# Kernel optimization log

Measured on AMD Instinct MI355X. Metric: run time of the kernel, lower is better.

The kernel has to match this reference:

```python
import jax, jax.numpy as jnp
import numpy as np

B, S, D, F, E, K = 2, 2048, 1024, 4096, 8, 2

def setup_inputs() -> dict:
    key = jax.random.key(0)
    ks = jax.random.split(key, 5)
    x = jax.random.normal(ks[0], (B, S, D), dtype=jnp.float32)
    Wg = jax.random.normal(ks[1], (D, E), dtype=jnp.float32) * 0.02   # gate (fp32)
    W1 = jax.random.normal(ks[2], (E, D, F), dtype=jnp.float32) * 0.02  # expert fc1
    b1 = jnp.zeros((E, F), dtype=jnp.float32)
    W2 = jax.random.normal(ks[3], (E, F, D), dtype=jnp.float32) * 0.02  # expert fc2
    b2 = jnp.zeros((E, D), dtype=jnp.float32)
    return {"x": x, "Wg": Wg, "W1": W1, "b1": b1, "W2": W2, "b2": b2}

def reference(x, Wg, W1, b1, W2, b2):
    b, s, d = x.shape
    e = Wg.shape[1]
    T = b * s
    C = (2 * K * T) // e  # generous capacity -> effectively no token drops
    xt = x.reshape(T, d)

    # --- top-2 gating (fp32) ---
    logits = xt.astype(jnp.float32) @ Wg.astype(jnp.float32)  # [T,E]
    gates = jax.nn.softmax(logits, axis=-1)
    idx1 = jnp.argmax(gates, axis=-1)                      # [T]
    mask1 = jax.nn.one_hot(idx1, e, dtype=gates.dtype)     # [T,E]
    gate1 = jnp.sum(gates * mask1, axis=-1)                # [T]
    logits2 = jnp.where(mask1 > 0, -jnp.inf, logits)
    idx2 = jnp.argmax(logits2, axis=-1)
    mask2 = jax.nn.one_hot(idx2, e, dtype=gates.dtype)
    gate2 = jnp.sum(gates * mask2, axis=-1)
    denom = gate1 + gate2 + 1e-9
    w1 = gate1 / denom
    w2 = gate2 / denom

    # --- capacity-based slot assignment (GShard-style) ---
    p1 = jnp.cumsum(mask1, axis=0) - mask1                 # earlier same-expert tokens
    pos1 = jnp.sum(p1 * mask1, axis=-1).astype(jnp.int32)  # [T]
    off = jnp.sum(mask1, axis=0)                           # [E] 1st-choice counts
    p2 = jnp.cumsum(mask2, axis=0) - mask2 + off[None, :]
    pos2 = jnp.sum(p2 * mask2, axis=-1).astype(jnp.int32)
    keep1 = (pos1 < C).astype(xt.dtype)
    keep2 = (pos2 < C).astype(xt.dtype)
    pos1 = jnp.clip(pos1, 0, C - 1)
    pos2 = jnp.clip(pos2, 0, C - 1)

    # --- dispatch (scatter tokens to expert slots) ---
    xe = jnp.zeros((e, C, d), dtype=xt.dtype)
    xe = xe.at[idx1, pos1].add(xt * keep1[:, None])
    xe = xe.at[idx2, pos2].add(xt * keep2[:, None])

    # --- grouped expert FFN: gelu(x W1 + b1) W2 + b2 ---
    h = jax.nn.gelu(jnp.einsum('ecd,edf->ecf', xe, W1) + b1[:, None, :], approximate=False)
    ye = jnp.einsum('ecf,efd->ecd', h, W2) + b2[:, None, :]  # [E,C,D]

    # --- combine (gather + weighted sum) ---
    out = ye[idx1, pos1] * (w1 * keep1)[:, None] + ye[idx2, pos2] * (w2 * keep2)[:, None]
    return out.reshape(b, s, d)
```

## Files before the change

kernel.cpp:

```cpp
#include <hip/hip_runtime.h>
#include <hip/hip_bf16.h>
#include <math.h>

#define Dv 1024
#define Fv 4096
#define Ev 8
#define Tt 4096
#define CAP 2048

typedef unsigned int u32;
typedef __bf16 bf16x8 __attribute__((ext_vector_type(8)));
typedef float f32x4 __attribute__((ext_vector_type(4)));

__device__ __forceinline__ unsigned short f2bf(float f) {
  u32 u = __float_as_uint(f);
  u32 r = (u + 0x7fffu + ((u >> 16) & 1u)) >> 16;
  return (unsigned short)r;
}

__device__ __forceinline__ void gload_lds16(const void* g, void* l) {
  __builtin_amdgcn_global_load_lds(
      (const __attribute__((address_space(1))) u32*)g,
      (__attribute__((address_space(3))) u32*)l, 16, 0, 0);
}

__global__ void __launch_bounds__(256)
transpose_bf16_kernel(const float* __restrict__ src, unsigned short* __restrict__ dst,
                      int R, int Cc) {
  __shared__ float tile[32][33];
  int e = blockIdx.z;
  src += (size_t)e * R * Cc;
  dst += (size_t)e * R * Cc;
  int c0 = blockIdx.x * 32, r0 = blockIdx.y * 32;
  int tx = threadIdx.x & 31, ty = threadIdx.x >> 5;
#pragma unroll
  for (int i = ty; i < 32; i += 8)
    tile[i][tx] = src[(size_t)(r0 + i) * Cc + (c0 + tx)];
  __syncthreads();
#pragma unroll
  for (int i = ty; i < 32; i += 8)
    dst[(size_t)(c0 + i) * R + (r0 + tx)] = f2bf(tile[tx][i]);
}

__global__ void __launch_bounds__(256)
gating_kernel(const float* __restrict__ x, const float* __restrict__ Wg,
              int* __restrict__ idx1, int* __restrict__ idx2,
              float* __restrict__ w1, float* __restrict__ w2) {
  int t = blockIdx.x * 4 + (threadIdx.x >> 6);
  int lane = threadIdx.x & 63;
  const float* xr = x + (size_t)t * Dv;
  float acc[Ev];
#pragma unroll
  for (int e = 0; e < Ev; ++e) acc[e] = 0.f;
#pragma unroll
  for (int j = 0; j < 4; ++j) {
    int dbase = (lane + 64 * j) * 4;
    float4 xv = *(const float4*)(xr + dbase);
    const float* wr = Wg + (size_t)dbase * Ev;
#pragma unroll
    for (int u = 0; u < 4; ++u) {
      float xd = (&xv.x)[u];
#pragma unroll
      for (int e = 0; e < Ev; ++e) acc[e] += xd * wr[u * Ev + e];
    }
  }
#pragma unroll
  for (int off = 32; off > 0; off >>= 1) {
#pragma unroll
    for (int e = 0; e < Ev; ++e) acc[e] += __shfl_xor(acc[e], off, 64);
  }
  if (lane == 0) {
    float mx = acc[0]; int i1 = 0;
#pragma unroll
    for (int e = 1; e < Ev; ++e) { if (acc[e] > mx) { mx = acc[e]; i1 = e; } }
    float ge[Ev]; float se = 0.f;
#pragma unroll
    for (int e = 0; e < Ev; ++e) { ge[e] = expf(acc[e] - mx); se += ge[e]; }
    float mx2 = -INFINITY; int i2 = 0; bool have = false;
#pragma unroll
    for (int e = 0; e < Ev; ++e) {
      if (e == i1) continue;
      if (!have || acc[e] > mx2) { mx2 = acc[e]; i2 = e; have = true; }
    }
    float g1 = 0.f, g2 = 0.f;
#pragma unroll
    for (int e = 0; e < Ev; ++e) { if (e == i1) g1 = ge[e]; if (e == i2) g2 = ge[e]; }
    g1 /= se; g2 /= se;
    float denom = g1 + g2 + 1e-9f;
    idx1[t] = i1; idx2[t] = i2;
    w1[t] = g1 / denom; w2[t] = g2 / denom;
  }
}

__global__ void __launch_bounds__(256)
scan_kernel(const int* __restrict__ gidx1, const int* __restrict__ gidx2,
            const float* __restrict__ gw1, const float* __restrict__ gw2,
            int* __restrict__ pos1, int* __restrict__ pos2,
            float* __restrict__ w1k, float* __restrict__ w2k,
            int* __restrict__ n_e) {
  __shared__ short s1[Tt], s2[Tt];
  __shared__ int c1[256][Ev], c2[256][Ev];
  __shared__ int tot1[Ev], tot2[Ev];
  int tid = threadIdx.x;
  for (int i = tid; i < Tt; i += 256) { s1[i] = (short)gidx1[i]; s2[i] = (short)gidx2[i]; }
  __syncthreads();
  int base = tid * 16;
  {
    int l1[Ev], l2[Ev];
#pragma unroll
    for (int e = 0; e < Ev; ++e) { l1[e] = 0; l2[e] = 0; }
    for (int j = 0; j < 16; ++j) {
      int a = s1[base + j], b = s2[base + j];
#pragma unroll
      for (int e = 0; e < Ev; ++e) { l1[e] += (a == e); l2[e] += (b == e); }
    }
#pragma unroll
    for (int e = 0; e < Ev; ++e) { c1[tid][e] = l1[e]; c2[tid][e] = l2[e]; }
  }
  __syncthreads();
  if (tid < Ev) {
    int run = 0;
    for (int c = 0; c < 256; ++c) { int v = c1[c][tid]; c1[c][tid] = run; run += v; }
    tot1[tid] = run;
  } else if (tid < 2 * Ev) {
    int e = tid - Ev; int run = 0;
    for (int c = 0; c < 256; ++c) { int v = c2[c][e]; c2[c][e] = run; run += v; }
    tot2[e] = run;
  }
  __syncthreads();
  if (tid < Ev) {
    int ne = tot1[tid] + tot2[tid];
    n_e[tid] = ne < CAP ? ne : CAP;
  }
  int r1[Ev], r2[Ev];
#pragma unroll
  for (int e = 0; e < Ev; ++e) { r1[e] = c1[tid][e]; r2[e] = c2[tid][e] + tot1[e]; }
  for (int j = 0; j < 16; ++j) {
    int tk = base + j;
    int e1 = s1[tk], e2 = s2[tk];
    int p1 = 0, p2 = 0;
#pragma unroll
    for (int e = 0; e < Ev; ++e) {
      if (e == e1) { p1 = r1[e]; r1[e]++; }
      if (e == e2) { p2 = r2[e]; r2[e]++; }
    }
    bool k1 = p1 < CAP, k2 = p2 < CAP;
    pos1[tk] = k1 ? p1 : -1;
    pos2[tk] = k2 ? p2 : -1;
    w1k[tk] = k1 ? gw1[tk] : 0.f;
    w2k[tk] = k2 ? gw2[tk] : 0.f;
  }
}

__global__ void __launch_bounds__(256)
dispatch_kernel(const float* __restrict__ x,
                const int* __restrict__ idx1, const int* __restrict__ idx2,
                const int* __restrict__ pos1, const int* __restrict__ pos2,
                unsigned short* __restrict__ Xe) {
  int t = blockIdx.x, tid = threadIdx.x;
  float4 xv = *(const float4*)(x + (size_t)t * Dv + tid * 4);
  ushort4 bv;
  bv.x = f2bf(xv.x); bv.y = f2bf(xv.y); bv.z = f2bf(xv.z); bv.w = f2bf(xv.w);
  int p1 = pos1[t], p2 = pos2[t];
  int e1 = idx1[t], e2 = idx2[t];
  if (p1 >= 0)
    *(ushort4*)(Xe + ((size_t)(e1 * CAP + p1)) * Dv + tid * 4) = bv;
  if (p2 >= 0)
    *(ushort4*)(Xe + ((size_t)(e2 * CAP + p2)) * Dv + tid * 4) = bv;
}

template <int MODE>
__global__ void __launch_bounds__(256, 2)
gemm_kernel(const unsigned short* __restrict__ A,
            const unsigned short* __restrict__ Bt,
            const float* __restrict__ bias,
            void* __restrict__ Out,
            const int* __restrict__ n_e,
            int M, int N, int K) {
  int e = blockIdx.z;
  int m0 = blockIdx.y * 128, n0 = blockIdx.x * 128;
  if (m0 >= n_e[e]) return;
  A += (size_t)e * M * K;
  Bt += (size_t)e * N * K;
  bias += (size_t)e * N;
  __shared__ unsigned short As[128 * 32];
  __shared__ unsigned short Bs[128 * 32];
  int tid = threadIdx.x;
  int wave = tid >> 6, lane = tid & 63;
  int wm = (wave & 1) * 64, wn = (wave >> 1) * 64;
  int quad = lane >> 4, lr = lane & 15;
  f32x4 acc[4][4];
#pragma unroll
  for (int i = 0; i < 4; ++i)
#pragma unroll
    for (int j = 0; j < 4; ++j)
#pragma unroll
      for (int r = 0; r < 4; ++r) acc[i][j][r] = 0.f;

  int srow = tid >> 2, scol = (tid & 3) * 8;
  const unsigned short* ga = A + (size_t)(m0 + srow) * K + scol;
  const unsigned short* gb = Bt + (size_t)(n0 + srow) * K + scol;
  unsigned short* la = &As[srow * 32 + scol];
  unsigned short* lb = &Bs[srow * 32 + scol];

  for (int k0 = 0; k0 < K; k0 += 32) {
    __syncthreads();
    gload_lds16(ga + k0, la);
    gload_lds16(ga + (size_t)64 * K + k0, la + 64 * 32);
    gload_lds16(gb + k0, lb);
    gload_lds16(gb + (size_t)64 * K + k0, lb + 64 * 32);
    __syncthreads();
    bf16x8 af[4], bfr[4];
#pragma unroll
    for (int mi = 0; mi < 4; ++mi)
      af[mi] = *(const bf16x8*)&As[(wm + mi * 16 + lr) * 32 + quad * 8];
#pragma unroll
    for (int ni = 0; ni < 4; ++ni)
      bfr[ni] = *(const bf16x8*)&Bs[(wn + ni * 16 + lr) * 32 + quad * 8];
#pragma unroll
    for (int mi = 0; mi < 4; ++mi)
#pragma unroll
      for (int ni = 0; ni < 4; ++ni)
        acc[mi][ni] = __builtin_amdgcn_mfma_f32_16x16x32_bf16(af[mi], bfr[ni], acc[mi][ni], 0, 0, 0);
  }

#pragma unroll
  for (int ni = 0; ni < 4; ++ni) {
    int col = n0 + wn + ni * 16 + lr;
    float bv = bias[col];
#pragma unroll
    for (int mi = 0; mi < 4; ++mi) {
#pragma unroll
      for (int r = 0; r < 4; ++r) {
        int row = m0 + wm + mi * 16 + quad * 4 + r;
        float v = acc[mi][ni][r] + bv;
        if (MODE == 0) {
          v = 0.5f * v * (1.0f + erff(v * 0.70710678118654752f));
          ((unsigned short*)Out)[((size_t)e * M + row) * N + col] = f2bf(v);
        } else {
          ((float*)Out)[((size_t)e * M + row) * N + col] = v;
        }
      }
    }
  }
}

__global__ void __launch_bounds__(256)
combine_kernel(const float* __restrict__ ye,
               const int* __restrict__ idx1, const int* __restrict__ idx2,
               const int* __restrict__ pos1, const int* __restrict__ pos2,
               const float* __restrict__ w1k, const float* __restrict__ w2k,
               float* __restrict__ out) {
  int t = blockIdx.x, tid = threadIdx.x;
  int p1 = pos1[t], p2 = pos2[t];
  float a1 = w1k[t], a2 = w2k[t];
  float4 o = make_float4(0.f, 0.f, 0.f, 0.f);
  if (p1 >= 0) {
    float4 y = *(const float4*)(ye + ((size_t)(idx1[t] * CAP + p1)) * Dv + tid * 4);
    o.x += a1 * y.x; o.y += a1 * y.y; o.z += a1 * y.z; o.w += a1 * y.w;
  }
  if (p2 >= 0) {
    float4 y = *(const float4*)(ye + ((size_t)(idx2[t] * CAP + p2)) * Dv + tid * 4);
    o.x += a2 * y.x; o.y += a2 * y.y; o.z += a2 * y.z; o.w += a2 * y.w;
  }
  *(float4*)(out + (size_t)t * Dv + tid * 4) = o;
}

extern "C" void kernel_launch(void* const* d_in, const int* in_sizes, int n_in,
                              void* d_out, int out_size, void* d_ws, size_t ws_size,
                              hipStream_t stream) {
  const float* x  = (const float*)d_in[0];
  const float* Wg = (const float*)d_in[1];
  const float* W1 = (const float*)d_in[2];
  const float* b1 = (const float*)d_in[3];
  const float* W2 = (const float*)d_in[4];
  const float* b2 = (const float*)d_in[5];
  float* out = (float*)d_out;

  char* p = (char*)d_ws;
  size_t off = 0;
  auto alloc = [&](size_t bytes) {
    void* q = p + off;
    off += (bytes + 255) & ~(size_t)255;
    return q;
  };
  unsigned short* Wt1 = (unsigned short*)alloc((size_t)Ev * Fv * Dv * 2);
  unsigned short* Wt2 = (unsigned short*)alloc((size_t)Ev * Dv * Fv * 2);
  unsigned short* Xe  = (unsigned short*)alloc((size_t)Ev * CAP * Dv * 2);
  unsigned short* h   = (unsigned short*)alloc((size_t)Ev * CAP * Fv * 2);
  int*   idx1 = (int*)alloc(Tt * 4);
  int*   idx2 = (int*)alloc(Tt * 4);
  int*   pos1 = (int*)alloc(Tt * 4);
  int*   pos2 = (int*)alloc(Tt * 4);
  float* w1   = (float*)alloc(Tt * 4);
  float* w2   = (float*)alloc(Tt * 4);
  float* w1k  = (float*)alloc(Tt * 4);
  float* w2k  = (float*)alloc(Tt * 4);
  int*   n_e  = (int*)alloc(Ev * 4);
  float* ye   = (float*)Wt1;

  transpose_bf16_kernel<<<dim3(Fv / 32, Dv / 32, Ev), 256, 0, stream>>>(W1, Wt1, Dv, Fv);
  transpose_bf16_kernel<<<dim3(Dv / 32, Fv / 32, Ev), 256, 0, stream>>>(W2, Wt2, Fv, Dv);
  gating_kernel<<<Tt / 4, 256, 0, stream>>>(x, Wg, idx1, idx2, w1, w2);
  scan_kernel<<<1, 256, 0, stream>>>(idx1, idx2, w1, w2, pos1, pos2, w1k, w2k, n_e);
  dispatch_kernel<<<Tt, 256, 0, stream>>>(x, idx1, idx2, pos1, pos2, Xe);
  gemm_kernel<0><<<dim3(Fv / 128, CAP / 128, Ev), 256, 0, stream>>>(
      Xe, Wt1, b1, h, n_e, CAP, Fv, Dv);
  gemm_kernel<1><<<dim3(Dv / 128, CAP / 128, Ev), 256, 0, stream>>>(
      h, Wt2, b2, ye, n_e, CAP, Dv, Fv);
  combine_kernel<<<Tt, 256, 0, stream>>>(ye, idx1, idx2, pos1, pos2, w1k, w2k, out);
}
```

Before: 678.5 us.

## Double GEMM K-tile to 64 with XOR-swizzled LDS and widen transpose tiles

The grouped GEMM now loads a 64-wide K slice per iteration, which halves the number of barrier pairs per K loop. It also XOR-swizzles the LDS column groups so the 128-byte rows avoid bank conflicts on fragment reads. The weight transpose kernel moves to 64x64 tiles and writes paired bf16 values as 32-bit stores, giving wider global writes. LDS use per block doubles to 32KB, which could affect occupancy with two blocks per CU.

New measurement: 622.0 us. 8.3% less time.

```diff
diff --git a/kernel.cpp b/kernel.cpp
--- a/kernel.cpp
+++ b/kernel.cpp
@@ -27,19 +27,25 @@
 __global__ void __launch_bounds__(256)
 transpose_bf16_kernel(const float* __restrict__ src, unsigned short* __restrict__ dst,
                       int R, int Cc) {
-  __shared__ float tile[32][33];
+  __shared__ float tile[64][65];
   int e = blockIdx.z;
   src += (size_t)e * R * Cc;
   dst += (size_t)e * R * Cc;
-  int c0 = blockIdx.x * 32, r0 = blockIdx.y * 32;
-  int tx = threadIdx.x & 31, ty = threadIdx.x >> 5;
-#pragma unroll
-  for (int i = ty; i < 32; i += 8)
-    tile[i][tx] = src[(size_t)(r0 + i) * Cc + (c0 + tx)];
+  int c0 = blockIdx.x * 64, r0 = blockIdx.y * 64;
+  int tc = threadIdx.x & 63, tr = threadIdx.x >> 6;
+#pragma unroll
+  for (int i = tr; i < 64; i += 4)
+    tile[i][tc] = src[(size_t)(r0 + i) * Cc + (c0 + tc)];
   __syncthreads();
-#pragma unroll
-  for (int i = ty; i < 32; i += 8)
-    dst[(size_t)(c0 + i) * R + (r0 + tx)] = f2bf(tile[tx][i]);
+  int rp = (threadIdx.x & 31) * 2, co = threadIdx.x >> 5;
+#pragma unroll
+  for (int k = 0; k < 8; ++k) {
+    int c = co + 8 * k;
+    ushort2 v;
+    v.x = f2bf(tile[rp][c]);
+    v.y = f2bf(tile[rp + 1][c]);
+    *(ushort2*)&dst[(size_t)(c0 + c) * R + (r0 + rp)] = v;
+  }
 }
 
 __global__ void __launch_bounds__(256)
@@ -183,12 +189,13 @@
   A += (size_t)e * M * K;
   Bt += (size_t)e * N * K;
   bias += (size_t)e * N;
-  __shared__ unsigned short As[128 * 32];
-  __shared__ unsigned short Bs[128 * 32];
+  __shared__ unsigned short As[128 * 64];
+  __shared__ unsigned short Bs[128 * 64];
   int tid = threadIdx.x;
   int wave = tid >> 6, lane = tid & 63;
   int wm = (wave & 1) * 64, wn = (wave >> 1) * 64;
   int quad = lane >> 4, lr = lane & 15;
+  int sw = lr & 7;
   f32x4 acc[4][4];
 #pragma unroll
   for (int i = 0; i < 4; ++i)
@@ -197,31 +204,43 @@
 #pragma unroll
       for (int r = 0; r < 4; ++r) acc[i][j][r] = 0.f;
 
-  int srow = tid >> 2, scol = (tid & 3) * 8;
-  const unsigned short* ga = A + (size_t)(m0 + srow) * K + scol;
-  const unsigned short* gb = Bt + (size_t)(n0 + srow) * K + scol;
-  unsigned short* la = &As[srow * 32 + scol];
-  unsigned short* lb = &Bs[srow * 32 + scol];
-
-  for (int k0 = 0; k0 < K; k0 += 32) {
+  int r_st = tid >> 3;
+  int g_st = tid & 7;
+  int gsrc = g_st ^ (r_st & 7);
+  const unsigned short* gA = A + (size_t)(m0 + r_st) * K + gsrc * 8;
+  const unsigned short* gB = Bt + (size_t)(n0 + r_st) * K + gsrc * 8;
+  unsigned short* lA = &As[tid * 8];
+  unsigned short* lB = &Bs[tid * 8];
+
+  for (int k0 = 0; k0 < K; k0 += 64) {
     __syncthreads();
-    gload_lds16(ga + k0, la);
-    gload_lds16(ga + (size_t)64 * K + k0, la + 64 * 32);
-    gload_lds16(gb + k0, lb);
-    gload_lds16(gb + (size_t)64 * K + k0, lb + 64 * 32);
+#pragma unroll
+    for (int s = 0; s < 4; ++s) {
+      gload_lds16(gA + (size_t)(s * 32) * K + k0, lA + s * 2048);
+      gload_lds16(gB + (size_t)(s * 32) * K + k0, lB + s * 2048);
+    }
     __syncthreads();
-    bf16x8 af[4], bfr[4];
-#pragma unroll
-    for (int mi = 0; mi < 4; ++mi)
-      af[mi] = *(const bf16x8*)&As[(wm + mi * 16 + lr) * 32 + quad * 8];
-#pragma unroll
-    for (int ni = 0; ni < 4; ++ni)
-      bfr[ni] = *(const bf16x8*)&Bs[(wn + ni * 16 + lr) * 32 + quad * 8];
-#pragma unroll
-    for (int mi = 0; mi < 4; ++mi)
-#pragma unroll
-      for (int ni = 0; ni < 4; ++ni)
-        acc[mi][ni] = __builtin_amdgcn_mfma_f32_16x16x32_bf16(af[mi], bfr[ni], acc[mi][ni], 0, 0, 0);
+#pragma unroll
+    for (int h = 0; h < 2; ++h) {
+      bf16x8 af[4], bfr[4];
+#pragma unroll
+      for (int mi = 0; mi < 4; ++mi) {
+        int row = wm + mi * 16 + lr;
+        int c = (h * 4 + quad) ^ sw;
+        af[mi] = *(const bf16x8*)&As[row * 64 + c * 8];
+      }
+#pragma unroll
+      for (int ni = 0; ni < 4; ++ni) {
+        int row = wn + ni * 16 + lr;
+        int c = (h * 4 + quad) ^ sw;
+        bfr[ni] = *(const bf16x8*)&Bs[row * 64 + c * 8];
+      }
+#pragma unroll
+      for (int mi = 0; mi < 4; ++mi)
+#pragma unroll
+        for (int ni = 0; ni < 4; ++ni)
+          acc[mi][ni] = __builtin_amdgcn_mfma_f32_16x16x32_bf16(af[mi], bfr[ni], acc[mi][ni], 0, 0, 0);
+    }
   }
 
 #pragma unroll
@@ -299,8 +318,8 @@
   int*   n_e  = (int*)alloc(Ev * 4);
   float* ye   = (float*)Wt1;
 
-  transpose_bf16_kernel<<<dim3(Fv / 32, Dv / 32, Ev), 256, 0, stream>>>(W1, Wt1, Dv, Fv);
-  transpose_bf16_kernel<<<dim3(Dv / 32, Fv / 32, Ev), 256, 0, stream>>>(W2, Wt2, Fv, Dv);
+  transpose_bf16_kernel<<<dim3(Fv / 64, Dv / 64, Ev), 256, 0, stream>>>(W1, Wt1, Dv, Fv);
+  transpose_bf16_kernel<<<dim3(Dv / 64, Fv / 64, Ev), 256, 0, stream>>>(W2, Wt2, Fv, Dv);
   gating_kernel<<<Tt / 4, 256, 0, stream>>>(x, Wg, idx1, idx2, w1, w2);
   scan_kernel<<<1, 256, 0, stream>>>(idx1, idx2, w1, w2, pos1, pos2, w1k, w2k, n_e);
   dispatch_kernel<<<Tt, 256, 0, stream>>>(x, idx1, idx2, pos1, pos2, Xe);
```
